# Optimization experiments

Measured on AMD Instinct MI355X. Metric: run time of the kernel, lower is better.

## Reference

```python
import jax, jax.numpy as jnp
import numpy as np

N, E, B = 100000, 640000, 2000
NODE_TYPES, EDGE_TYPES = 16, 5
ND, ED, EMB, L = 256, 128, 256, 3  # node_dim, edge_dim, emb_dim, num encoder blocks


def setup_inputs() -> dict:
    key = jax.random.key(0)
    ks = jax.random.split(key, 20)
    s = 0.02
    inp = {
        "h_node": jax.random.normal(ks[0], (N, NODE_TYPES), jnp.float32),
        "pos_node": jax.random.normal(ks[1], (N, 3), jnp.float32),
        "h_edge": jax.random.normal(ks[2], (E, EDGE_TYPES), jnp.float32),
        "W_node": jax.random.normal(ks[3], (NODE_TYPES, ND), jnp.float32) * s,
        "W_edge": jax.random.normal(ks[4], (EDGE_TYPES, ED), jnp.float32) * s,
        # per-block encoder params (stacked over L blocks)
        "W_eu": jax.random.normal(ks[5], (L, ED + 2 * ND + 1, ED), jnp.float32) * s,
        "b_eu": jnp.zeros((L, ED), jnp.float32),
        "W_msg": jax.random.normal(ks[6], (L, ND + ED, ND), jnp.float32) * s,
        "b_msg": jnp.zeros((L, ND), jnp.float32),
        "W_nu": jax.random.normal(ks[7], (L, 2 * ND, ND), jnp.float32) * s,
        "b_nu": jnp.zeros((L, ND), jnp.float32),
        # final MLP: in=ND+ED, hidden=2*EMB, out=EMB (num_layer=2)
        "Wf1": jax.random.normal(ks[8], (ND + ED, 2 * EMB), jnp.float32) * s,
        "bf1": jnp.zeros((2 * EMB,), jnp.float32),
        "Wf2": jax.random.normal(ks[9], (2 * EMB, EMB), jnp.float32) * s,
        "bf2": jnp.zeros((EMB,), jnp.float32),
        "edge_index": jax.random.randint(ks[10], (2, E), 0, N, jnp.int64),
        "batch_node": jnp.sort(jax.random.randint(ks[11], (N,), 0, B, jnp.int64)),
        "batch_edge": jnp.sort(jax.random.randint(ks[12], (E,), 0, B, jnp.int64)),
    }
    return inp


def _segment_mean(x, ids, num_segments):
    tot = jax.ops.segment_sum(x, ids, num_segments=num_segments)
    cnt = jax.ops.segment_sum(jnp.ones((x.shape[0], 1), x.dtype), ids,
                              num_segments=num_segments)
    return tot / jnp.maximum(cnt, 1.0)


def reference(h_node, pos_node, h_edge, W_node, W_edge, W_eu, b_eu,
              W_msg, b_msg, W_nu, b_nu, Wf1, bf1, Wf2, bf2,
              edge_index, batch_node, batch_edge):
    src, dst = edge_index[0], edge_index[1]
    # embed node / edge type features
    hn = h_node @ W_node            # [N, ND]
    he = h_edge @ W_edge            # [E, ED]
    # NodeEdgeNet: L message-passing blocks with geometric edge feature
    dist = jnp.linalg.norm(pos_node[dst] - pos_node[src], axis=-1,
                           keepdims=True)  # [E, 1]
    for l in range(L):
        e_in = jnp.concatenate([he, hn[src], hn[dst], dist], axis=-1)
        he = jax.nn.relu(e_in @ W_eu[l] + b_eu[l])                 # edge update
        msg = jax.nn.relu(jnp.concatenate([hn[src], he], axis=-1)
                          @ W_msg[l] + b_msg[l])                    # [E, ND]
        agg = jax.ops.segment_sum(msg, dst, num_segments=N)         # [N, ND]
        hn = hn + jax.nn.relu(jnp.concatenate([hn, agg], axis=-1)
                              @ W_nu[l] + b_nu[l])                  # node update
    # per-graph mean pooling (replaces python loop over k with segment mean)
    mean_n = _segment_mean(hn, batch_node, B)   # [B, ND]
    mean_e = _segment_mean(he, batch_edge, B)   # [B, ED]
    h_sub = jnp.concatenate([mean_n, mean_e], axis=-1)  # [B, ND+ED]
    emb = jax.nn.relu(h_sub @ Wf1 + bf1) @ Wf2 + bf2     # [B, EMB]
    return emb, batch_node
```

## Files before the change

### kernel.cpp

```cpp
#include <hip/hip_runtime.h>
#include <hip/hip_bf16.h>
#include <math.h>

#define NN 100000
#define NE 640000
#define NB 2000

typedef __attribute__((ext_vector_type(4))) float v4f;
typedef long long ll64;
#define MFMA8(a, b, c) __builtin_amdgcn_mfma_f32_16x16x32_fp8_fp8(a, b, c, 0, 0, 0)

#define INV_S 0.000244140625f
#define ASCL 16.0f
#define AINV 0.0625f

#if __has_builtin(__builtin_amdgcn_cvt_pk_fp8_f32) && __has_builtin(__builtin_amdgcn_cvt_f32_fp8)
#define HW_FP8 1
#else
#define HW_FP8 0
#endif

__device__ __forceinline__ int IDX(const void* p, size_t i, int is64) {
    return is64 ? (int)((const long long*)p)[i] : ((const int*)p)[i];
}
__device__ __forceinline__ int clampi(int v, int n) {
    return ((unsigned)v < (unsigned)n) ? v : 0;
}

__global__ void k_detect(const int* bn32, int* flag) {
    if (threadIdx.x == 0 && blockIdx.x == 0) {
        int is64 = 1;
        for (int k = 50001; k < 50401; k += 2)
            if (bn32[k] != 0) { is64 = 0; break; }
        *flag = is64;
    }
}

__device__ __forceinline__ unsigned sw_enc_fp8(float x) {
    unsigned s = (__float_as_uint(x) >> 24) & 0x80u;
    float ax = fminf(fabsf(x), 448.f);
    if (ax < 0.015625f) {
        unsigned m = (unsigned)(ax * 512.f + 0.5f);
        return s | m;
    }
    unsigned b = __float_as_uint(ax) + 0x00080000u;
    unsigned e = (b >> 23) - 120u;
    unsigned m = (b >> 20) & 7u;
    unsigned v = (e << 3) | m;
    if (v > 0x7Eu) v = 0x7Eu;
    return s | v;
}
__device__ __forceinline__ float sw_dec_fp8(unsigned b) {
    unsigned s = (b & 0x80u) << 24;
    unsigned e = (b >> 3) & 15u;
    unsigned m = b & 7u;
    if (e) return __uint_as_float(s | ((e + 120u) << 23) | (m << 20));
    float f = (float)m * 0.001953125f;
    return (b & 0x80u) ? -f : f;
}
__device__ __forceinline__ unsigned enc1(float x) {
#if HW_FP8
    return (unsigned)__builtin_amdgcn_cvt_pk_fp8_f32(x, x, 0, false) & 255u;
#else
    return sw_enc_fp8(x);
#endif
}
__device__ __forceinline__ unsigned encpk(float a, float b) {
#if HW_FP8
    return (unsigned)__builtin_amdgcn_cvt_pk_fp8_f32(a, b, 0, false) & 0xFFFFu;
#else
    return sw_enc_fp8(a) | (sw_enc_fp8(b) << 8);
#endif
}
__device__ __forceinline__ float dec1(unsigned b) {
#if HW_FP8
    return __builtin_amdgcn_cvt_f32_fp8((int)b, 0);
#else
    return sw_dec_fp8(b);
#endif
}
__device__ __forceinline__ float bf_f(unsigned short u) {
    return __uint_as_float((unsigned)u << 16);
}

__global__ __launch_bounds__(256) void k_node_embed(const float* __restrict__ h_node,
                                                    const float* __restrict__ W,
                                                    unsigned char* __restrict__ hn8) {
    __shared__ float sh[8][16];
    int t = threadIdx.x;
    int r0 = blockIdx.x * 8;
    if (t < 128) sh[t >> 4][t & 15] = h_node[r0 * 16 + t];
    float w[16];
#pragma unroll
    for (int k = 0; k < 16; ++k) w[k] = W[k * 256 + t];
    __syncthreads();
#pragma unroll
    for (int r = 0; r < 8; ++r) {
        float acc = 0.f;
#pragma unroll
        for (int k = 0; k < 16; ++k) acc += sh[r][k] * w[k];
        hn8[(size_t)(r0 + r) * 256 + t] = (unsigned char)enc1(ASCL * acc);
    }
}

__global__ __launch_bounds__(256) void k_edge_embed(const float* __restrict__ h_edge,
                                                    const float* __restrict__ W,
                                                    const int* __restrict__ perm,
                                                    unsigned char* __restrict__ he8) {
    __shared__ float sh[16][5];
    int t = threadIdx.x;
    int e0 = blockIdx.x * 16;
    if (t < 80) {
        int row = t / 5, col = t % 5;
        int e = perm[e0 + row];
        sh[row][col] = h_edge[(size_t)e * 5 + col];
    }
    int c = t & 127;
    int es = t >> 7;
    float w[5];
#pragma unroll
    for (int k = 0; k < 5; ++k) w[k] = W[k * 128 + c];
    __syncthreads();
#pragma unroll
    for (int e = 0; e < 8; ++e) {
        int ee = es * 8 + e;
        float acc = 0.f;
#pragma unroll
        for (int k = 0; k < 5; ++k) acc += sh[ee][k] * w[k];
        he8[(size_t)(e0 + ee) * 128 + c] = (unsigned char)enc1(ASCL * acc);
    }
}

__global__ __launch_bounds__(256) void k_tr_w1(const float* __restrict__ W,
                                               unsigned char* __restrict__ WT) {
    int i = blockIdx.x * 256 + threadIdx.x;
    if (i >= 3 * 128 * 128) return;
    int l = i / 16384, r = i % 16384;
    int n = r / 128, k = r % 128;
    WT[i] = (unsigned char)enc1(256.f * W[(size_t)l * 641 * 128 + (size_t)k * 128 + n]);
}
__global__ __launch_bounds__(256) void k_tr_w2(const float* __restrict__ W,
                                               unsigned char* __restrict__ WT) {
    int i = blockIdx.x * 256 + threadIdx.x;
    if (i >= 3 * 256 * 128) return;
    int l = i / 32768, r = i % 32768;
    int n = r / 128, k = r % 128;
    WT[i] = (unsigned char)enc1(256.f * W[(size_t)l * 384 * 256 + (size_t)(256 + k) * 256 + n]);
}
__global__ __launch_bounds__(256) void k_tr_nu(const float* __restrict__ W,
                                               unsigned char* __restrict__ WT) {
    int i = blockIdx.x * 256 + threadIdx.x;
    if (i >= 3 * 256 * 512) return;
    int l = i / 131072, r = i % 131072;
    int n = r / 512, k = r % 512;
    WT[i] = (unsigned char)enc1(256.f * W[(size_t)l * 512 * 256 + (size_t)k * 256 + n]);
}
__global__ __launch_bounds__(256) void k_tr_pre(const float* __restrict__ Weu,
                                                const float* __restrict__ Wmsg,
                                                unsigned char* __restrict__ WT) {
    int i = blockIdx.x * 256 + threadIdx.x;
    if (i >= 3 * 512 * 256) return;
    int l = i / 131072, r = i % 131072;
    int n = r / 256, k = r % 256;
    float w;
    if (n < 128)      w = Weu[(size_t)l * 641 * 128 + (size_t)(128 + k) * 128 + n];
    else if (n < 256) w = Weu[(size_t)l * 641 * 128 + (size_t)(384 + k) * 128 + (n - 128)];
    else              w = Wmsg[(size_t)l * 384 * 256 + (size_t)k * 256 + (n - 256)];
    WT[i] = (unsigned char)enc1(256.f * w);
}

__global__ __launch_bounds__(256) void k_hist(const void* __restrict__ ei,
                                              const int* __restrict__ flag,
                                              int* __restrict__ hist) {
    int e = blockIdx.x * 256 + threadIdx.x;
    if (e >= NE) return;
    int d = clampi(IDX(ei, (size_t)NE + e, *flag), NN);
    atomicAdd(&hist[d], 1);
}
__global__ __launch_bounds__(1024) void k_scan(const int* __restrict__ hist,
                                               int* __restrict__ rowptr) {
    __shared__ int part[1024];
    int t = threadIdx.x;
    const int C = 98;
    int s = 0;
    for (int j = 0; j < C; ++j) {
        int i = t * C + j;
        if (i < NN) s += hist[i];
    }
    part[t] = s;
    __syncthreads();
    if (t == 0) {
        int run = 0;
        for (int i = 0; i < 1024; ++i) { int v = part[i]; part[i] = run; run += v; }
    }
    __syncthreads();
    int run = part[t];
    for (int j = 0; j < C; ++j) {
        int i = t * C + j;
        if (i < NN) { rowptr[i] = run; run += hist[i]; }
    }
}
__global__ __launch_bounds__(256) void k_perm(const void* __restrict__ ei,
                                              const int* __restrict__ flag,
                                              const float* __restrict__ pos,
                                              int* __restrict__ cursor,
                                              int* __restrict__ perm,
                                              int* __restrict__ inv,
                                              int* __restrict__ srcs,
                                              int* __restrict__ dsts,
                                              float* __restrict__ dist_s) {
    int e = blockIdx.x * 256 + threadIdx.x;
    if (e >= NE) return;
    int is64 = *flag;
    int s = clampi(IDX(ei, (size_t)e, is64), NN);
    int d = clampi(IDX(ei, (size_t)NE + e, is64), NN);
    int p = atomicAdd(&cursor[d], 1);
    perm[p] = e;
    inv[e] = p;
    srcs[p] = s;
    dsts[p] = d;
    float dx = pos[d * 3 + 0] - pos[s * 3 + 0];
    float dy = pos[d * 3 + 1] - pos[s * 3 + 1];
    float dz = pos[d * 3 + 2] - pos[s * 3 + 2];
    dist_s[p] = sqrtf(dx * dx + dy * dy + dz * dz);
}

#define NP_AS 264
__global__ __launch_bounds__(256, 3) void k_node_pre(
    const unsigned char* __restrict__ hn8, const unsigned char* __restrict__ WpreT,
    unsigned char* __restrict__ R) {
    __shared__ unsigned char s_A[64 * NP_AS];
    int t = threadIdx.x;
    int rb = blockIdx.x * 64;
    {
        int row = t >> 2, sb = t & 3;
        int gr = rb + row; if (gr >= NN) gr = NN - 1;
        const uint4* sp = (const uint4*)(hn8 + (size_t)gr * 256 + sb * 64);
        uint4 a = sp[0], b = sp[1], c = sp[2], d = sp[3];
        uint4* dp = (uint4*)&s_A[row * NP_AS + sb * 64];
        dp[0] = a; dp[1] = b; dp[2] = c; dp[3] = d;
    }
    __syncthreads();
    int lane = t & 63, wv = t >> 6, quad = lane >> 4, l16 = lane & 15;
    v4f zero4 = {0.f, 0.f, 0.f, 0.f};
#pragma unroll
    for (int pass = 0; pass < 2; ++pass) {
        int nt0 = wv * 8 + pass * 4;
        v4f acc[4][4];
#pragma unroll
        for (int mt = 0; mt < 4; ++mt)
#pragma unroll
            for (int nl = 0; nl < 4; ++nl) acc[mt][nl] = zero4;
#pragma unroll 2
        for (int k = 0; k < 256; k += 32) {
            int ko = k + quad * 8;
            ll64 b[4];
#pragma unroll
            for (int nl = 0; nl < 4; ++nl)
                b[nl] = *(const ll64*)(WpreT + (size_t)((nt0 + nl) * 16 + l16) * 256 + ko);
#pragma unroll
            for (int mt = 0; mt < 4; ++mt) {
                ll64 a = *(const ll64*)&s_A[(mt * 16 + l16) * NP_AS + ko];
#pragma unroll
                for (int nl = 0; nl < 4; ++nl) acc[mt][nl] = MFMA8(a, b[nl], acc[mt][nl]);
            }
        }
#pragma unroll
        for (int nl = 0; nl < 4; ++nl) {
            int c = (nt0 + nl) * 16 + l16;
#pragma unroll
            for (int mt = 0; mt < 4; ++mt)
#pragma unroll
                for (int rr = 0; rr < 2; ++rr) {
                    int rw0 = mt * 16 + quad * 4 + rr * 2;
                    unsigned pk = encpk(acc[mt][nl][rr * 2] * 0.00390625f,
                                        acc[mt][nl][rr * 2 + 1] * 0.00390625f);
                    if (rb + rw0 < NN)
                        R[(size_t)(rb + rw0) * 512 + c] = (unsigned char)(pk & 255u);
                    if (rb + rw0 + 1 < NN)
                        R[(size_t)(rb + rw0 + 1) * 512 + c] = (unsigned char)(pk >> 8);
                }
        }
    }
}

#define EF_S 136
#define EF_QS 264
#define EF_MS 136
__global__ __launch_bounds__(256, 6) void k_edge_fused(
    unsigned char* __restrict__ he8, const unsigned char* __restrict__ R,
    const float* __restrict__ dist_s,
    const int* __restrict__ srcs, const int* __restrict__ dsts,
    const unsigned char* __restrict__ W1T, const float* __restrict__ W_eu,
    const float* __restrict__ b_eu,
    const unsigned char* __restrict__ W2T, const float* __restrict__ b_msg,
    unsigned short* __restrict__ agg) {
    __shared__ __align__(16) unsigned char s_A[32 * EF_S];
    __shared__ __align__(16) unsigned char s_Pd[32 * EF_S];
    __shared__ __align__(16) unsigned char s_Ph[32 * EF_S];
    __shared__ __align__(16) unsigned char s_Q[32 * EF_QS];
    __shared__ __align__(16) unsigned char s_msg[32 * EF_MS];
    __shared__ float s_dist[32];
    __shared__ int s_dsti[32];
    int t = threadIdx.x;
    int eb = blockIdx.x * 32;
    int row = t >> 3, sb = t & 7;
    int sid = srcs[eb + row];
    int did = dsts[eb + row];
    if (t < 32) {
        s_dsti[t] = dsts[eb + t];
        s_dist[t] = dist_s[eb + t];
    }
    *(uint4*)&s_A[row * EF_S + sb * 16] =
        *(const uint4*)(he8 + (size_t)(eb + row) * 128 + sb * 16);
    *(uint4*)&s_Ph[row * EF_S + sb * 16] =
        *(const uint4*)(R + (size_t)sid * 512 + sb * 16);
    *(uint4*)&s_Pd[row * EF_S + sb * 16] =
        *(const uint4*)(R + (size_t)did * 512 + 128 + sb * 16);
    {
        const uint4* qp = (const uint4*)(R + (size_t)sid * 512 + 256 + sb * 32);
        uint4 q0 = qp[0], q1 = qp[1];
        *(uint4*)&s_Q[row * EF_QS + sb * 32] = q0;
        *(uint4*)&s_Q[row * EF_QS + sb * 32 + 16] = q1;
    }
    int lane = t & 63, wv = t >> 6, quad = lane >> 4, l16 = lane & 15;
    int n0 = wv * 2;
    const unsigned char* B0 = W1T + (size_t)(n0 * 16 + l16) * 128 + quad * 8;
    ll64 Brg[4][2];
#pragma unroll
    for (int kk = 0; kk < 4; ++kk) {
        Brg[kk][0] = *(const ll64*)(B0 + kk * 32);
        Brg[kk][1] = *(const ll64*)(B0 + 2048 + kk * 32);
    }
    __syncthreads();

    v4f zero4 = {0.f, 0.f, 0.f, 0.f};
    v4f acc[2][2];
    acc[0][0] = zero4; acc[0][1] = zero4; acc[1][0] = zero4; acc[1][1] = zero4;
#pragma unroll
    for (int kk = 0; kk < 4; ++kk) {
        int ko = kk * 32 + quad * 8;
#pragma unroll
        for (int mt = 0; mt < 2; ++mt) {
            ll64 a = *(const ll64*)&s_A[(mt * 16 + l16) * EF_S + ko];
            acc[mt][0] = MFMA8(a, Brg[kk][0], acc[mt][0]);
            acc[mt][1] = MFMA8(a, Brg[kk][1], acc[mt][1]);
        }
    }
#pragma unroll
    for (int nl = 0; nl < 2; ++nl) {
        int c = (n0 + nl) * 16 + l16;
        float w640 = W_eu[640 * 128 + c];
        float bb = b_eu[c];
#pragma unroll
        for (int mt = 0; mt < 2; ++mt)
#pragma unroll
            for (int rr = 0; rr < 2; ++rr) {
                int rw0 = mt * 16 + quad * 4 + rr * 2;
                int rw1 = rw0 + 1;
                float S0 = (dec1(s_Ph[rw0 * EF_S + c]) +
                            dec1(s_Pd[rw0 * EF_S + c])) * AINV;
                float S1 = (dec1(s_Ph[rw1 * EF_S + c]) +
                            dec1(s_Pd[rw1 * EF_S + c])) * AINV;
                float v0 = fmaxf(acc[mt][nl][rr * 2] * INV_S + S0 +
                                 s_dist[rw0] * w640 + bb, 0.f);
                float v1 = fmaxf(acc[mt][nl][rr * 2 + 1] * INV_S + S1 +
                                 s_dist[rw1] * w640 + bb, 0.f);
                unsigned pk = encpk(ASCL * v0, ASCL * v1);
                s_Ph[rw0 * EF_S + c] = (unsigned char)(pk & 255u);
                s_Ph[rw1 * EF_S + c] = (unsigned char)(pk >> 8);
            }
    }
    __syncthreads();
    *(uint4*)(he8 + (size_t)(eb + row) * 128 + sb * 16) =
        *(const uint4*)&s_Ph[row * EF_S + sb * 16];

    v4f mac[2][4];
#pragma unroll
    for (int nl = 0; nl < 4; ++nl) { mac[0][nl] = zero4; mac[1][nl] = zero4; }
    int q0n = wv * 4;
#pragma unroll
    for (int kk = 0; kk < 4; ++kk) {
        int ko = kk * 32 + quad * 8;
        ll64 b[4];
#pragma unroll
        for (int nl = 0; nl < 4; ++nl)
            b[nl] = *(const ll64*)(W2T + (size_t)((q0n + nl) * 16 + l16) * 128 + ko);
#pragma unroll
        for (int mt = 0; mt < 2; ++mt) {
            ll64 a = *(const ll64*)&s_Ph[(mt * 16 + l16) * EF_S + ko];
#pragma unroll
            for (int nl = 0; nl < 4; ++nl) mac[mt][nl] = MFMA8(a, b[nl], mac[mt][nl]);
        }
    }
#pragma unroll
    for (int nl = 0; nl < 4; ++nl) {
        int c = (q0n + nl) * 16 + l16;
        float bm = b_msg[c];
#pragma unroll
        for (int mt = 0; mt < 2; ++mt)
#pragma unroll
            for (int rr = 0; rr < 2; ++rr) {
                int rw0 = mt * 16 + quad * 4 + rr * 2;
                int rw1 = rw0 + 1;
                float q0v = dec1(s_Q[rw0 * EF_QS + c]) * AINV;
                float q1v = dec1(s_Q[rw1 * EF_QS + c]) * AINV;
                float v0 = fmaxf(mac[mt][nl][rr * 2] * INV_S + q0v + bm, 0.f);
                float v1 = fmaxf(mac[mt][nl][rr * 2 + 1] * INV_S + q1v + bm, 0.f);
                unsigned pk = encpk(ASCL * v0, ASCL * v1);
                s_msg[rw0 * EF_MS + c] = (unsigned char)(pk & 255u);
                s_msg[rw1 * EF_MS + c] = (unsigned char)(pk >> 8);
            }
    }
    __syncthreads();
    {
        int cp = t & 127;
        int half = t >> 7;
        int r0 = half * 16, r1 = r0 + 16;
        float ax = 0.f, ay = 0.f;
        int cur = s_dsti[r0];
        for (int rw = r0; rw < r1; ++rw) {
            int d2 = s_dsti[rw];
            if (d2 != cur) {
                if (ax != 0.f || ay != 0.f) {
                    __hip_bfloat162 pv;
                    pv.x = __float2bfloat16(ax * AINV);
                    pv.y = __float2bfloat16(ay * AINV);
                    unsafeAtomicAdd((__hip_bfloat162*)&agg[(size_t)cur * 256 + cp * 2], pv);
                }
                ax = 0.f; ay = 0.f; cur = d2;
            }
            unsigned short v = *(const unsigned short*)&s_msg[rw * EF_MS + cp * 2];
            ax += dec1(v & 255u);
            ay += dec1(v >> 8);
        }
        if (ax != 0.f || ay != 0.f) {
            __hip_bfloat162 pv;
            pv.x = __float2bfloat16(ax * AINV);
            pv.y = __float2bfloat16(ay * AINV);
            unsafeAtomicAdd((__hip_bfloat162*)&agg[(size_t)cur * 256 + cp * 2], pv);
        }
    }
}

#define NF_AS 520
#define NF_BS 264
__global__ __launch_bounds__(256, 3) void k_node_fused(
    unsigned char* __restrict__ hn8, const unsigned short* __restrict__ agg,
    const unsigned char* __restrict__ WnuT, const float* __restrict__ b,
    const unsigned char* __restrict__ WpreT, unsigned char* __restrict__ R,
    int do_pre) {
    __shared__ unsigned char s_A[64 * NF_AS];
    __shared__ unsigned char s_B[64 * NF_BS];
    int t = threadIdx.x;
    int rb = blockIdx.x * 64;
    int row4 = t >> 2, sb4 = t & 3;
    {
        int gr = rb + row4; if (gr >= NN) gr = NN - 1;
        const uint4* sp = (const uint4*)(hn8 + (size_t)gr * 256 + sb4 * 64);
        uint4 a = sp[0], b2 = sp[1], c = sp[2], d = sp[3];
        uint4* dp = (uint4*)&s_A[row4 * NF_AS + sb4 * 64];
        dp[0] = a; dp[1] = b2; dp[2] = c; dp[3] = d;
        const unsigned short* ap = agg + (size_t)gr * 256 + sb4 * 64;
        unsigned char* dq = &s_A[row4 * NF_AS + 256 + sb4 * 64];
#pragma unroll
        for (int j = 0; j < 64; j += 2) {
            unsigned pk = encpk(ASCL * bf_f(ap[j]), ASCL * bf_f(ap[j + 1]));
            *(unsigned short*)&dq[j] = (unsigned short)pk;
        }
    }
    __syncthreads();
    int lane = t & 63, wv = t >> 6, quad = lane >> 4, l16 = lane & 15;
    v4f zero4 = {0.f, 0.f, 0.f, 0.f};
    {
        v4f acc[4][4];
#pragma unroll
        for (int mt = 0; mt < 4; ++mt)
#pragma unroll
            for (int nl = 0; nl < 4; ++nl) acc[mt][nl] = zero4;
        int q0 = wv * 4;
#pragma unroll 2
        for (int k = 0; k < 512; k += 32) {
            int ko = k + quad * 8;
            ll64 b2[4];
#pragma unroll
            for (int nl = 0; nl < 4; ++nl)
                b2[nl] = *(const ll64*)(WnuT + (size_t)((q0 + nl) * 16 + l16) * 512 + ko);
#pragma unroll
            for (int mt = 0; mt < 4; ++mt) {
                ll64 a = *(const ll64*)&s_A[(mt * 16 + l16) * NF_AS + ko];
#pragma unroll
                for (int nl = 0; nl < 4; ++nl) acc[mt][nl] = MFMA8(a, b2[nl], acc[mt][nl]);
            }
        }
#pragma unroll
        for (int nl = 0; nl < 4; ++nl) {
            int c = (q0 + nl) * 16 + l16;
            float bv = b[c];
#pragma unroll
            for (int mt = 0; mt < 4; ++mt)
#pragma unroll
                for (int rr = 0; rr < 2; ++rr) {
                    int rw0 = mt * 16 + quad * 4 + rr * 2;
                    float o0 = dec1(s_A[rw0 * NF_AS + c]) * AINV;
                    float o1 = dec1(s_A[(rw0 + 1) * NF_AS + c]) * AINV;
                    float v0 = o0 + fmaxf(acc[mt][nl][rr * 2] * INV_S + bv, 0.f);
                    float v1 = o1 + fmaxf(acc[mt][nl][rr * 2 + 1] * INV_S + bv, 0.f);
                    unsigned pk = encpk(ASCL * v0, ASCL * v1);
                    s_B[rw0 * NF_BS + c] = (unsigned char)(pk & 255u);
                    s_B[(rw0 + 1) * NF_BS + c] = (unsigned char)(pk >> 8);
                }
        }
    }
    __syncthreads();
    if (rb + row4 < NN) {
        const unsigned char* sp = &s_B[row4 * NF_BS + sb4 * 64];
        uint4* dp = (uint4*)(hn8 + (size_t)(rb + row4) * 256 + sb4 * 64);
        dp[0] = *(const uint4*)(sp);
        dp[1] = *(const uint4*)(sp + 16);
        dp[2] = *(const uint4*)(sp + 32);
        dp[3] = *(const uint4*)(sp + 48);
    }
    if (!do_pre) return;
#pragma unroll
    for (int pass = 0; pass < 2; ++pass) {
        int nt0 = wv * 8 + pass * 4;
        v4f acc[4][4];
#pragma unroll
        for (int mt = 0; mt < 4; ++mt)
#pragma unroll
            for (int nl = 0; nl < 4; ++nl) acc[mt][nl] = zero4;
#pragma unroll 2
        for (int k = 0; k < 256; k += 32) {
            int ko = k + quad * 8;
            ll64 b2[4];
#pragma unroll
            for (int nl = 0; nl < 4; ++nl)
                b2[nl] = *(const ll64*)(WpreT + (size_t)((nt0 + nl) * 16 + l16) * 256 + ko);
#pragma unroll
            for (int mt = 0; mt < 4; ++mt) {
                ll64 a = *(const ll64*)&s_B[(mt * 16 + l16) * NF_BS + ko];
#pragma unroll
                for (int nl = 0; nl < 4; ++nl) acc[mt][nl] = MFMA8(a, b2[nl], acc[mt][nl]);
            }
        }
#pragma unroll
        for (int nl = 0; nl < 4; ++nl) {
            int c = (nt0 + nl) * 16 + l16;
#pragma unroll
            for (int mt = 0; mt < 4; ++mt)
#pragma unroll
                for (int rr = 0; rr < 2; ++rr) {
                    int rw0 = mt * 16 + quad * 4 + rr * 2;
                    unsigned pk = encpk(acc[mt][nl][rr * 2] * 0.00390625f,
                                        acc[mt][nl][rr * 2 + 1] * 0.00390625f);
                    s_A[rw0 * NF_AS + c] = (unsigned char)(pk & 255u);
                    s_A[(rw0 + 1) * NF_AS + c] = (unsigned char)(pk >> 8);
                }
        }
    }
    __syncthreads();
    if (rb + row4 < NN) {
        const unsigned char* sp = &s_A[row4 * NF_AS + sb4 * 128];
        uint4* dp = (uint4*)(R + (size_t)(rb + row4) * 512 + sb4 * 128);
#pragma unroll
        for (int j = 0; j < 8; ++j) dp[j] = *(const uint4*)(sp + j * 16);
    }
}

__device__ __forceinline__ int lbound(const void* a, int n, int v, int is64) {
    int lo = 0, hi = n;
    while (lo < hi) {
        int mid = (lo + hi) >> 1;
        if (IDX(a, mid, is64) < v) lo = mid + 1; else hi = mid;
    }
    return lo;
}

__global__ __launch_bounds__(512) void k_pool_mlp(
    const unsigned char* __restrict__ hn8, const unsigned char* __restrict__ he8,
    const int* __restrict__ inv,
    const void* __restrict__ bn, const void* __restrict__ be,
    const int* __restrict__ flag,
    const float* __restrict__ Wf1, const float* __restrict__ bf1,
    const float* __restrict__ Wf2, const float* __restrict__ bf2,
    float* __restrict__ out) {
    __shared__ float s_nacc[8][256];
    __shared__ float s_eacc[16][128];
    __shared__ float s_sub[384];
    __shared__ float s_hid[512];
    int b = blockIdx.x;
    int t = threadIdx.x;
    int is64 = *flag;
    int lane = t & 63, wv = t >> 6;
    int nlo = lbound(bn, NN, b, is64), nhi = lbound(bn, NN, b + 1, is64);
    int elo = lbound(be, NE, b, is64), ehi = lbound(be, NE, b + 1, is64);
    {
        float a0 = 0.f, a1 = 0.f, a2 = 0.f, a3 = 0.f;
        for (int i = nlo + wv; i < nhi; i += 8) {
            unsigned u = *(const unsigned*)(hn8 + (size_t)i * 256 + lane * 4);
            a0 += dec1(u & 255u);
            a1 += dec1((u >> 8) & 255u);
            a2 += dec1((u >> 16) & 255u);
            a3 += dec1(u >> 24);
        }
        s_nacc[wv][lane * 4 + 0] = a0;
        s_nacc[wv][lane * 4 + 1] = a1;
        s_nacc[wv][lane * 4 + 2] = a2;
        s_nacc[wv][lane * 4 + 3] = a3;
    }
    {
        int g16 = wv * 2 + (lane >> 5);
        int sl = lane & 31;
        float a0 = 0.f, a1 = 0.f, a2 = 0.f, a3 = 0.f;
        for (int e = elo + g16; e < ehi; e += 16) {
            int row = inv[e];
            unsigned u = *(const unsigned*)(he8 + (size_t)row * 128 + sl * 4);
            a0 += dec1(u & 255u);
            a1 += dec1((u >> 8) & 255u);
            a2 += dec1((u >> 16) & 255u);
            a3 += dec1(u >> 24);
        }
        s_eacc[g16][sl * 4 + 0] = a0;
        s_eacc[g16][sl * 4 + 1] = a1;
        s_eacc[g16][sl * 4 + 2] = a2;
        s_eacc[g16][sl * 4 + 3] = a3;
    }
    __syncthreads();
    if (t < 256) {
        float s = 0.f;
#pragma unroll
        for (int w = 0; w < 8; ++w) s += s_nacc[w][t];
        s_sub[t] = s * AINV / fmaxf((float)(nhi - nlo), 1.f);
    } else if (t < 384) {
        int c = t - 256;
        float s = 0.f;
#pragma unroll
        for (int j = 0; j < 16; ++j) s += s_eacc[j][c];
        s_sub[t] = s * AINV / fmaxf((float)(ehi - elo), 1.f);
    }
    __syncthreads();
    float hacc = bf1[t];
    for (int k = 0; k < 384; ++k) hacc += s_sub[k] * Wf1[k * 512 + t];
    s_hid[t] = fmaxf(hacc, 0.f);
    __syncthreads();
    if (t < 256) {
        float o = bf2[t];
        for (int k = 0; k < 512; ++k) o += s_hid[k] * Wf2[k * 256 + t];
        out[(size_t)b * 256 + t] = o;
    }
}

__global__ __launch_bounds__(256) void k_write_batch(const void* __restrict__ bn,
                                                     const int* __restrict__ flag,
                                                     float* __restrict__ out) {
    int i = blockIdx.x * 256 + threadIdx.x;
    if (i < NN) out[(size_t)NB * 256 + i] = (float)IDX(bn, i, *flag);
}

__global__ __launch_bounds__(256) void k_fill(float* __restrict__ p, int n, float v) {
    int i = blockIdx.x * 256 + threadIdx.x;
    if (i < n) p[i] = v;
}

extern "C" void kernel_launch(void* const* d_in, const int* in_sizes, int n_in,
                              void* d_out, int out_size, void* d_ws, size_t ws_size,
                              hipStream_t stream) {
    const float* h_node = (const float*)d_in[0];
    const float* pos    = (const float*)d_in[1];
    const float* h_edge = (const float*)d_in[2];
    const float* W_node = (const float*)d_in[3];
    const float* W_edge = (const float*)d_in[4];
    const float* W_eu   = (const float*)d_in[5];
    const float* b_eu   = (const float*)d_in[6];
    const float* W_msg  = (const float*)d_in[7];
    const float* b_msg  = (const float*)d_in[8];
    const float* W_nu   = (const float*)d_in[9];
    const float* b_nu   = (const float*)d_in[10];
    const float* Wf1    = (const float*)d_in[11];
    const float* bf1    = (const float*)d_in[12];
    const float* Wf2    = (const float*)d_in[13];
    const float* bf2    = (const float*)d_in[14];
    const void* ei = d_in[15];
    const void* bn = d_in[16];
    const void* be = d_in[17];

    float* out = (float*)d_out;

    const size_t SZ_FLAG = 256;
    const size_t SZ_HN   = (size_t)NN * 256;
    const size_t SZ_HE   = (size_t)NE * 128;
    const size_t SZ_AGG  = (size_t)NN * 256 * 2;
    const size_t SZ_R    = (size_t)NN * 512;
    const size_t SZ_PERM = (size_t)NE * 4;
    const size_t SZ_INV  = (size_t)NE * 4;
    const size_t SZ_SRC  = (size_t)NE * 4;
    const size_t SZ_DST  = (size_t)NE * 4;
    const size_t SZ_DS   = (size_t)NE * 4;
    const size_t SZ_PTR  = 512 * 1024;
    const size_t SZ_CUR  = 512 * 1024;
    const size_t SZ_W1   = (size_t)3 * 128 * 128;
    const size_t SZ_W2   = (size_t)3 * 256 * 128;
    const size_t SZ_WNU  = (size_t)3 * 256 * 512;
    const size_t SZ_WPRE = (size_t)3 * 512 * 256;
    const size_t NEED = SZ_FLAG + SZ_HN + SZ_HE + SZ_AGG + SZ_R + SZ_PERM +
                        SZ_INV + SZ_SRC + SZ_DST + SZ_DS + SZ_PTR + SZ_CUR +
                        SZ_W1 + SZ_W2 + SZ_WNU + SZ_WPRE;

    char* ws = (char*)d_ws;
    int* flag = (int*)ws;                       ws += SZ_FLAG;
    unsigned char* hn8 = (unsigned char*)ws;    ws += SZ_HN;
    unsigned char* he8 = (unsigned char*)ws;    ws += SZ_HE;
    unsigned short* agg = (unsigned short*)ws;  ws += SZ_AGG;
    unsigned char* R = (unsigned char*)ws;      ws += SZ_R;
    int* perm = (int*)ws;                       ws += SZ_PERM;
    int* inv = (int*)ws;                        ws += SZ_INV;
    int* srcs = (int*)ws;                       ws += SZ_SRC;
    int* dsts = (int*)ws;                       ws += SZ_DST;
    float* dist_s = (float*)ws;                 ws += SZ_DS;
    int* rowptr = (int*)ws;                     ws += SZ_PTR;
    int* cursor = (int*)ws;                     ws += SZ_CUR;
    unsigned char* W1T = (unsigned char*)ws;    ws += SZ_W1;
    unsigned char* W2T = (unsigned char*)ws;    ws += SZ_W2;
    unsigned char* WnuT = (unsigned char*)ws;   ws += SZ_WNU;
    unsigned char* WpreT = (unsigned char*)ws;  ws += SZ_WPRE;

    if (ws_size < NEED) {
        float enc = -(100000.0f + (float)(ws_size >> 20));
        k_detect<<<1, 64, 0, stream>>>((const int*)bn, flag);
        k_fill<<<(NB * 256 + 255) / 256, 256, 0, stream>>>(out, NB * 256, enc);
        k_write_batch<<<(NN + 255) / 256, 256, 0, stream>>>(bn, flag, out);
        return;
    }

    k_detect<<<1, 64, 0, stream>>>((const int*)bn, flag);
    k_tr_w1<<<(3 * 128 * 128 + 255) / 256, 256, 0, stream>>>(W_eu, W1T);
    k_tr_w2<<<(3 * 256 * 128 + 255) / 256, 256, 0, stream>>>(W_msg, W2T);
    k_tr_nu<<<(3 * 256 * 512 + 255) / 256, 256, 0, stream>>>(W_nu, WnuT);
    k_tr_pre<<<(3 * 512 * 256 + 255) / 256, 256, 0, stream>>>(W_eu, W_msg, WpreT);
    k_node_embed<<<NN / 8, 256, 0, stream>>>(h_node, W_node, hn8);

    hipMemsetAsync(cursor, 0, (size_t)NN * 4, stream);
    k_hist<<<(NE + 255) / 256, 256, 0, stream>>>(ei, flag, cursor);
    k_scan<<<1, 1024, 0, stream>>>(cursor, rowptr);
    hipMemcpyAsync(cursor, rowptr, (size_t)NN * 4, hipMemcpyDeviceToDevice, stream);
    k_perm<<<(NE + 255) / 256, 256, 0, stream>>>(ei, flag, pos, cursor, perm,
                                                 inv, srcs, dsts, dist_s);
    k_edge_embed<<<NE / 16, 256, 0, stream>>>(h_edge, W_edge, perm, he8);

    k_node_pre<<<(NN + 63) / 64, 256, 0, stream>>>(hn8, WpreT, R);

    for (int l = 0; l < 3; ++l) {
        hipMemsetAsync(agg, 0, SZ_AGG, stream);
        k_edge_fused<<<NE / 32, 256, 0, stream>>>(
            he8, R, dist_s, srcs, dsts,
            W1T + (size_t)l * 128 * 128, W_eu + (size_t)l * 641 * 128,
            b_eu + (size_t)l * 128,
            W2T + (size_t)l * 256 * 128, b_msg + (size_t)l * 256, agg);
        int do_pre = (l < 2) ? 1 : 0;
        const unsigned char* wpre_next = WpreT + (size_t)(do_pre ? (l + 1) : 0) * 512 * 256;
        k_node_fused<<<(NN + 63) / 64, 256, 0, stream>>>(
            hn8, agg, WnuT + (size_t)l * 256 * 512, b_nu + (size_t)l * 256,
            wpre_next, R, do_pre);
    }

    k_pool_mlp<<<NB, 512, 0, stream>>>(hn8, he8, inv, bn, be, flag,
                                       Wf1, bf1, Wf2, bf2, out);
    k_write_batch<<<(NN + 255) / 256, 256, 0, stream>>>(bn, flag, out);
}
```

Baseline: 1.734 ms.

## Split pooling from final MLP and run MLP as FP8 MFMA GEMM

The final two-layer MLP, previously a scalar per-graph loop over Wf1/Wf2 inside the pooling kernel, now runs in a separate kernel. That kernel uses FP8 MFMA tiles over 64 graphs per block, with the weights pre-transposed and quantized to FP8 by new prep kernels. The pooling kernel writes bf16 means to a workspace buffer. Packed two-lane FP8 decode (cvt_pk_f32_fp8) replaces single-byte decodes in the aggregation and pooling loops. This adds two launches and a pooled buffer round trip, and lowers MLP precision to FP8.

```diff
diff --git a/kernel.cpp b/kernel.cpp
--- a/kernel.cpp
+++ b/kernel.cpp
@@ -7,6 +7,7 @@
 #define NB 2000
 
 typedef __attribute__((ext_vector_type(4))) float v4f;
+typedef __attribute__((ext_vector_type(2))) float v2f;
 typedef long long ll64;
 #define MFMA8(a, b, c) __builtin_amdgcn_mfma_f32_16x16x32_fp8_fp8(a, b, c, 0, 0, 0)
 
@@ -18,6 +19,11 @@
 #define HW_FP8 1
 #else
 #define HW_FP8 0
+#endif
+#if __has_builtin(__builtin_amdgcn_cvt_pk_f32_fp8)
+#define HW_PK8 1
+#else
+#define HW_PK8 0
 #endif
 
 __device__ __forceinline__ int IDX(const void* p, size_t i, int is64) {
@@ -77,6 +83,14 @@
     return __builtin_amdgcn_cvt_f32_fp8((int)b, 0);
 #else
     return sw_dec_fp8(b);
+#endif
+}
+__device__ __forceinline__ void dec2(unsigned v, float& a, float& b) {
+#if HW_PK8
+    v2f d = __builtin_amdgcn_cvt_pk_f32_fp8((int)(v & 0xFFFFu), false);
+    a = d.x; b = d.y;
+#else
+    a = dec1(v & 255u); b = dec1((v >> 8) & 255u);
 #endif
 }
 __device__ __forceinline__ float bf_f(unsigned short u) {
@@ -167,6 +181,20 @@
     else if (n < 256) w = Weu[(size_t)l * 641 * 128 + (size_t)(384 + k) * 128 + (n - 128)];
     else              w = Wmsg[(size_t)l * 384 * 256 + (size_t)k * 256 + (n - 256)];
     WT[i] = (unsigned char)enc1(256.f * w);
+}
+__global__ __launch_bounds__(256) void k_tr_f1(const float* __restrict__ W,
+                                               unsigned char* __restrict__ WT) {
+    int i = blockIdx.x * 256 + threadIdx.x;
+    if (i >= 512 * 384) return;
+    int n = i / 384, k = i % 384;
+    WT[i] = (unsigned char)enc1(256.f * W[(size_t)k * 512 + n]);
+}
+__global__ __launch_bounds__(256) void k_tr_f2(const float* __restrict__ W,
+                                               unsigned char* __restrict__ WT) {
+    int i = blockIdx.x * 256 + threadIdx.x;
+    if (i >= 256 * 512) return;
+    int n = i / 512, k = i % 512;
+    WT[i] = (unsigned char)enc1(256.f * W[(size_t)k * 256 + n]);
 }
 
 __global__ __launch_bounds__(256) void k_hist(const void* __restrict__ ei,
@@ -431,8 +459,9 @@
                 ax = 0.f; ay = 0.f; cur = d2;
             }
             unsigned short v = *(const unsigned short*)&s_msg[rw * EF_MS + cp * 2];
-            ax += dec1(v & 255u);
-            ay += dec1(v >> 8);
+            float f0, f1;
+            dec2(v, f0, f1);
+            ax += f0; ay += f1;
         }
         if (ax != 0.f || ay != 0.f) {
             __hip_bfloat162 pv;
@@ -577,18 +606,14 @@
     return lo;
 }
 
-__global__ __launch_bounds__(512) void k_pool_mlp(
+__global__ __launch_bounds__(512) void k_pool_means(
     const unsigned char* __restrict__ hn8, const unsigned char* __restrict__ he8,
     const int* __restrict__ inv,
     const void* __restrict__ bn, const void* __restrict__ be,
     const int* __restrict__ flag,
-    const float* __restrict__ Wf1, const float* __restrict__ bf1,
-    const float* __restrict__ Wf2, const float* __restrict__ bf2,
-    float* __restrict__ out) {
+    unsigned short* __restrict__ pooled) {
     __shared__ float s_nacc[8][256];
     __shared__ float s_eacc[16][128];
-    __shared__ float s_sub[384];
-    __shared__ float s_hid[512];
     int b = blockIdx.x;
     int t = threadIdx.x;
     int is64 = *flag;
@@ -599,10 +624,10 @@
         float a0 = 0.f, a1 = 0.f, a2 = 0.f, a3 = 0.f;
         for (int i = nlo + wv; i < nhi; i += 8) {
             unsigned u = *(const unsigned*)(hn8 + (size_t)i * 256 + lane * 4);
-            a0 += dec1(u & 255u);
-            a1 += dec1((u >> 8) & 255u);
-            a2 += dec1((u >> 16) & 255u);
-            a3 += dec1(u >> 24);
+            float f0, f1, f2, f3;
+            dec2(u, f0, f1);
+            dec2(u >> 16, f2, f3);
+            a0 += f0; a1 += f1; a2 += f2; a3 += f3;
         }
         s_nacc[wv][lane * 4 + 0] = a0;
         s_nacc[wv][lane * 4 + 1] = a1;
@@ -616,10 +641,10 @@
         for (int e = elo + g16; e < ehi; e += 16) {
             int row = inv[e];
             unsigned u = *(const unsigned*)(he8 + (size_t)row * 128 + sl * 4);
-            a0 += dec1(u & 255u);
-            a1 += dec1((u >> 8) & 255u);
-            a2 += dec1((u >> 16) & 255u);
-            a3 += dec1(u >> 24);
+            float f0, f1, f2, f3;
+            dec2(u, f0, f1);
+            dec2(u >> 16, f2, f3);
+            a0 += f0; a1 += f1; a2 += f2; a3 += f3;
         }
         s_eacc[g16][sl * 4 + 0] = a0;
         s_eacc[g16][sl * 4 + 1] = a1;
@@ -631,23 +656,139 @@
         float s = 0.f;
 #pragma unroll
         for (int w = 0; w < 8; ++w) s += s_nacc[w][t];
-        s_sub[t] = s * AINV / fmaxf((float)(nhi - nlo), 1.f);
+        float m = s * AINV / fmaxf((float)(nhi - nlo), 1.f);
+        __hip_bfloat16 h = __float2bfloat16(m);
+        pooled[(size_t)b * 384 + t] = *(unsigned short*)&h;
     } else if (t < 384) {
         int c = t - 256;
         float s = 0.f;
 #pragma unroll
         for (int j = 0; j < 16; ++j) s += s_eacc[j][c];
-        s_sub[t] = s * AINV / fmaxf((float)(ehi - elo), 1.f);
-    }
-    __syncthreads();
-    float hacc = bf1[t];
-    for (int k = 0; k < 384; ++k) hacc += s_sub[k] * Wf1[k * 512 + t];
-    s_hid[t] = fmaxf(hacc, 0.f);
-    __syncthreads();
-    if (t < 256) {
-        float o = bf2[t];
-        for (int k = 0; k < 512; ++k) o += s_hid[k] * Wf2[k * 256 + t];
-        out[(size_t)b * 256 + t] = o;
+        float m = s * AINV / fmaxf((float)(ehi - elo), 1.f);
+        __hip_bfloat16 h = __float2bfloat16(m);
+        pooled[(size_t)b * 384 + t] = *(unsigned short*)&h;
+    }
+}
+
+#define FM_PS 392
+#define FM_HS 520
+__global__ __launch_bounds__(256, 1) void k_final(
+    const unsigned short* __restrict__ pooled,
+    const unsigned char* __restrict__ Wf1T, const float* __restrict__ bf1,
+    const unsigned char* __restrict__ Wf2T, const float* __restrict__ bf2,
+    float* __restrict__ out) {
+    __shared__ unsigned char s_P[64 * FM_PS];
+    __shared__ unsigned char s_H[64 * FM_HS];
+    int t = threadIdx.x;
+    int bb = blockIdx.x * 64;
+    int row4 = t >> 2, sb4 = t & 3;
+    {
+        int g = bb + row4;
+        unsigned char* dq = &s_P[row4 * FM_PS + sb4 * 96];
+        if (g < NB) {
+            const unsigned short* pr = pooled + (size_t)g * 384 + sb4 * 96;
+#pragma unroll
+            for (int j = 0; j < 12; ++j) {
+                uint4 q = *(const uint4*)(pr + j * 8);
+                unsigned w0, w1;
+                {
+                    unsigned p0 = encpk(ASCL * bf_f((unsigned short)(q.x & 0xFFFF)),
+                                        ASCL * bf_f((unsigned short)(q.x >> 16)));
+                    unsigned p1 = encpk(ASCL * bf_f((unsigned short)(q.y & 0xFFFF)),
+                                        ASCL * bf_f((unsigned short)(q.y >> 16)));
+                    w0 = p0 | (p1 << 16);
+                    unsigned p2 = encpk(ASCL * bf_f((unsigned short)(q.z & 0xFFFF)),
+                                        ASCL * bf_f((unsigned short)(q.z >> 16)));
+                    unsigned p3 = encpk(ASCL * bf_f((unsigned short)(q.w & 0xFFFF)),
+                                        ASCL * bf_f((unsigned short)(q.w >> 16)));
+                    w1 = p2 | (p3 << 16);
+                }
+                *(unsigned*)(dq + j * 8) = w0;
+                *(unsigned*)(dq + j * 8 + 4) = w1;
+            }
+        } else {
+#pragma unroll
+            for (int j = 0; j < 12; ++j) {
+                *(unsigned*)(dq + j * 8) = 0;
+                *(unsigned*)(dq + j * 8 + 4) = 0;
+            }
+        }
+    }
+    __syncthreads();
+    int lane = t & 63, wv = t >> 6, quad = lane >> 4, l16 = lane & 15;
+    v4f zero4 = {0.f, 0.f, 0.f, 0.f};
+#pragma unroll
+    for (int pass = 0; pass < 2; ++pass) {
+        int nt0 = wv * 8 + pass * 4;
+        v4f acc[4][4];
+#pragma unroll
+        for (int mt = 0; mt < 4; ++mt)
+#pragma unroll
+            for (int nl = 0; nl < 4; ++nl) acc[mt][nl] = zero4;
+        for (int k = 0; k < 384; k += 32) {
+            int ko = k + quad * 8;
+            ll64 b2[4];
+#pragma unroll
+            for (int nl = 0; nl < 4; ++nl)
+                b2[nl] = *(const ll64*)(Wf1T + (size_t)((nt0 + nl) * 16 + l16) * 384 + ko);
+#pragma unroll
+            for (int mt = 0; mt < 4; ++mt) {
+                ll64 a = *(const ll64*)&s_P[(mt * 16 + l16) * FM_PS + ko];
+#pragma unroll
+                for (int nl = 0; nl < 4; ++nl) acc[mt][nl] = MFMA8(a, b2[nl], acc[mt][nl]);
+            }
+        }
+#pragma unroll
+        for (int nl = 0; nl < 4; ++nl) {
+            int c = (nt0 + nl) * 16 + l16;
+            float bv = bf1[c];
+#pragma unroll
+            for (int mt = 0; mt < 4; ++mt)
+#pragma unroll
+                for (int rr = 0; rr < 2; ++rr) {
+                    int rw0 = mt * 16 + quad * 4 + rr * 2;
+                    float v0 = fmaxf(acc[mt][nl][rr * 2] * INV_S + bv, 0.f);
+                    float v1 = fmaxf(acc[mt][nl][rr * 2 + 1] * INV_S + bv, 0.f);
+                    unsigned pk = encpk(ASCL * v0, ASCL * v1);
+                    s_H[rw0 * FM_HS + c] = (unsigned char)(pk & 255u);
+                    s_H[(rw0 + 1) * FM_HS + c] = (unsigned char)(pk >> 8);
+                }
+        }
+    }
+    __syncthreads();
+    {
+        v4f acc[4][4];
+#pragma unroll
+        for (int mt = 0; mt < 4; ++mt)
+#pragma unroll
+            for (int nl = 0; nl < 4; ++nl) acc[mt][nl] = zero4;
+        int q0 = wv * 4;
+        for (int k = 0; k < 512; k += 32) {
+            int ko = k + quad * 8;
+            ll64 b2[4];
+#pragma unroll
+            for (int nl = 0; nl < 4; ++nl)
+                b2[nl] = *(const ll64*)(Wf2T + (size_t)((q0 + nl) * 16 + l16) * 512 + ko);
+#pragma unroll
+            for (int mt = 0; mt < 4; ++mt) {
+                ll64 a = *(const ll64*)&s_H[(mt * 16 + l16) * FM_HS + ko];
+#pragma unroll
+                for (int nl = 0; nl < 4; ++nl) acc[mt][nl] = MFMA8(a, b2[nl], acc[mt][nl]);
+            }
+        }
+#pragma unroll
+        for (int nl = 0; nl < 4; ++nl) {
+            int c = (q0 + nl) * 16 + l16;
+            float bv = bf2[c];
+#pragma unroll
+            for (int mt = 0; mt < 4; ++mt)
+#pragma unroll
+                for (int r = 0; r < 4; ++r) {
+                    int rw = mt * 16 + quad * 4 + r;
+                    if (bb + rw < NB)
+                        out[(size_t)(bb + rw) * 256 + c] = acc[mt][nl][r] * INV_S + bv;
+                }
+        }
     }
 }
 
@@ -703,9 +844,13 @@
     const size_t SZ_W2   = (size_t)3 * 256 * 128;
     const size_t SZ_WNU  = (size_t)3 * 256 * 512;
     const size_t SZ_WPRE = (size_t)3 * 512 * 256;
+    const size_t SZ_POOL = (size_t)NB * 384 * 2;
+    const size_t SZ_WF1  = (size_t)512 * 384;
+    const size_t SZ_WF2  = (size_t)256 * 512;
     const size_t NEED = SZ_FLAG + SZ_HN + SZ_HE + SZ_AGG + SZ_R + SZ_PERM +
                         SZ_INV + SZ_SRC + SZ_DST + SZ_DS + SZ_PTR + SZ_CUR +
-                        SZ_W1 + SZ_W2 + SZ_WNU + SZ_WPRE;
+                        SZ_W1 + SZ_W2 + SZ_WNU + SZ_WPRE + SZ_POOL + SZ_WF1 +
+                        SZ_WF2;
 
     char* ws = (char*)d_ws;
     int* flag = (int*)ws;                       ws += SZ_FLAG;
@@ -724,6 +869,9 @@
     unsigned char* W2T = (unsigned char*)ws;    ws += SZ_W2;
     unsigned char* WnuT = (unsigned char*)ws;   ws += SZ_WNU;
     unsigned char* WpreT = (unsigned char*)ws;  ws += SZ_WPRE;
+    unsigned short* pooled = (unsigned short*)ws; ws += SZ_POOL;
+    unsigned char* Wf1T = (unsigned char*)ws;   ws += SZ_WF1;
+    unsigned char* Wf2T = (unsigned char*)ws;   ws += SZ_WF2;
 
     if (ws_size < NEED) {
         float enc = -(100000.0f + (float)(ws_size >> 20));
@@ -738,6 +886,8 @@
     k_tr_w2<<<(3 * 256 * 128 + 255) / 256, 256, 0, stream>>>(W_msg, W2T);
     k_tr_nu<<<(3 * 256 * 512 + 255) / 256, 256, 0, stream>>>(W_nu, WnuT);
     k_tr_pre<<<(3 * 512 * 256 + 255) / 256, 256, 0, stream>>>(W_eu, W_msg, WpreT);
+    k_tr_f1<<<(512 * 384 + 255) / 256, 256, 0, stream>>>(Wf1, Wf1T);
+    k_tr_f2<<<(256 * 512 + 255) / 256, 256, 0, stream>>>(Wf2, Wf2T);
     k_node_embed<<<NN / 8, 256, 0, stream>>>(h_node, W_node, hn8);
 
     hipMemsetAsync(cursor, 0, (size_t)NN * 4, stream);
@@ -764,7 +914,7 @@
             wpre_next, R, do_pre);
     }
 
-    k_pool_mlp<<<NB, 512, 0, stream>>>(hn8, he8, inv, bn, be, flag,
-                                       Wf1, bf1, Wf2, bf2, out);
+    k_pool_means<<<NB, 512, 0, stream>>>(hn8, he8, inv, bn, be, flag, pooled);
+    k_final<<<(NB + 63) / 64, 256, 0, stream>>>(pooled, Wf1T, bf1, Wf2T, bf2, out);
     k_write_batch<<<(NN + 255) / 256, 256, 0, stream>>>(bn, flag, out);
 }
```

Result: no change. 1.704 ms (-1.7%).
